# Kernel tuning notes

Measured on AMD Instinct MI355X. Metric: run time of the kernel, lower is better.

Reference implementation:

```python
import math
import jax, jax.numpy as jnp
import numpy as np

N_HEADS = 16

def setup_inputs() -> dict:
    key = jax.random.key(0)
    k1, k2, k3 = jax.random.split(key, 3)
    B, T, C = 2, 2048, 1024
    x = jax.random.normal(k1, (B, T, C), dtype=jnp.float32)
    # Linear weights stored as [in, out] so y = x @ W + b (same math as torch Linear)
    w_qkv = jax.random.normal(k2, (C, 3 * C), dtype=jnp.float32) * (1.0 / math.sqrt(C))
    b_qkv = jnp.zeros((3 * C,), dtype=jnp.float32)
    w_out = jax.random.normal(k3, (C, C), dtype=jnp.float32) * (1.0 / math.sqrt(C))
    b_out = jnp.zeros((C,), dtype=jnp.float32)
    return {"x": x, "w_qkv": w_qkv, "b_qkv": b_qkv, "w_out": w_out, "b_out": b_out}

def reference(x, w_qkv, b_qkv, w_out, b_out):
    B, T, C = x.shape
    H = N_HEADS
    hd = C // H
    qkv = (x @ w_qkv + b_qkv).reshape(B, T, 3, H, hd)
    q, k, v = qkv[:, :, 0], qkv[:, :, 1], qkv[:, :, 2]  # [B,T,H,hd]
    scale = 1.0 / math.sqrt(hd)
    att = jnp.einsum('bqhd,bkhd->bhqk', q, k) * scale  # [B,H,T,T]
    causal = jnp.tril(jnp.ones((T, T), dtype=bool))
    att = jnp.where(causal[None, None], att, jnp.float32(-jnp.inf))
    att = jax.nn.softmax(att, axis=-1)
    # dropout p=0.0 -> identity (eval mode)
    y = jnp.einsum('bhqk,bkhd->bqhd', att, v).reshape(B, T, C)
    return y @ w_out + b_out
```

## Files before the change

kernel.cpp:

```cpp
#include <hip/hip_runtime.h>
#include <hip/hip_bf16.h>
#include <stdint.h>


typedef __bf16 bf16_t;
typedef __attribute__((ext_vector_type(8))) __bf16 bf16x8;
typedef __attribute__((ext_vector_type(4))) __bf16 bf16x4;
typedef __attribute__((ext_vector_type(4))) short short4v;
typedef __attribute__((ext_vector_type(4))) float f32x4;

static_assert(sizeof(bf16x8) == 16, "bf16x8 must be 16B");

#if defined(__has_builtin)
#if __has_builtin(__builtin_amdgcn_mfma_f32_16x16x16bf16_1k)
#define HAVE_MFMA16 1
#endif
#if __has_builtin(__builtin_amdgcn_exp2f)
#define EXP2F(x) __builtin_amdgcn_exp2f(x)
#endif
#endif
#ifndef HAVE_MFMA16
#define HAVE_MFMA16 0
#endif
#ifndef EXP2F
#define EXP2F(x) exp2f(x)
#endif

__device__ inline void async_copy16(const bf16_t* gsrc, bf16_t* lds_dst) {
  __builtin_amdgcn_global_load_lds(
      (const __attribute__((address_space(1))) uint32_t*)(const void*)gsrc,
      (__attribute__((address_space(3))) uint32_t*)(void*)lds_dst,
      16, 0, 0);
}

__global__ __launch_bounds__(256) void prep_kernel(
    const float* __restrict__ x, const float* __restrict__ wq,
    const float* __restrict__ wo, bf16_t* __restrict__ xb,
    bf16_t* __restrict__ wqkvT, bf16_t* __restrict__ woutT) {
  __shared__ bf16_t tile[32][33];
  const int bid = blockIdx.x;
  if (bid < 2048) {
    const int i = bid * 256 + threadIdx.x;
    const float4* s = (const float4*)x;
    float4 a = s[i * 2], b = s[i * 2 + 1];
    bf16x8 o;
    o[0] = (bf16_t)a.x; o[1] = (bf16_t)a.y; o[2] = (bf16_t)a.z; o[3] = (bf16_t)a.w;
    o[4] = (bf16_t)b.x; o[5] = (bf16_t)b.y; o[6] = (bf16_t)b.z; o[7] = (bf16_t)b.w;
    ((bf16x8*)xb)[i] = o;
    return;
  }
  const bool isq = bid < 5120;
  const int id = isq ? bid - 2048 : bid - 5120;
  const int C = isq ? 3072 : 1024;
  const int R = 1024;
  const int nbx = isq ? 96 : 32;
  const float* in = isq ? wq : wo;
  bf16_t* out = isq ? wqkvT : woutT;
  const int c0 = (id % nbx) * 32, r0 = (id / nbx) * 32;
  const int tx4 = threadIdx.x & 7;
  const int ty = threadIdx.x >> 3;
  {
    const float4 ld =
        *(const float4*)&in[(size_t)(r0 + ty) * C + c0 + tx4 * 4];
    tile[ty][tx4 * 4 + 0] = (bf16_t)ld.x;
    tile[ty][tx4 * 4 + 1] = (bf16_t)ld.y;
    tile[ty][tx4 * 4 + 2] = (bf16_t)ld.z;
    tile[ty][tx4 * 4 + 3] = (bf16_t)ld.w;
  }
  __syncthreads();
  {
    bf16x4 w;
    w[0] = tile[tx4 * 4 + 0][ty];
    w[1] = tile[tx4 * 4 + 1][ty];
    w[2] = tile[tx4 * 4 + 2][ty];
    w[3] = tile[tx4 * 4 + 3][ty];
    *(bf16x4*)&out[(size_t)(c0 + ty) * R + r0 + tx4 * 4] = w;
  }
}

template <bool OUT_F32>
__global__ __launch_bounds__(256, 3) void gemm_bt_kernel(
    const bf16_t* __restrict__ A, const bf16_t* __restrict__ Bt,
    const float* __restrict__ bias, void* __restrict__ Cv, int M, int N,
    int K) {
  __shared__ __align__(16) bf16_t sA[128 * 64];
  __shared__ __align__(16) bf16_t sB[128 * 64];
  const int tid = threadIdx.x;
  const int wave = tid >> 6, lane = tid & 63;
  const int quad = lane >> 4, l16 = lane & 15;
  const int wm = (wave >> 1) * 64, wn = (wave & 1) * 64;
  const int bm = blockIdx.y * 128, bn = blockIdx.x * 128;

  const int rl = lane >> 3, cl = lane & 7;
  const int srow = wave * 32;
  const bf16_t* gA =
      A + (size_t)(bm + srow + rl) * K + (size_t)((cl ^ rl) << 3);
  const bf16_t* gB =
      Bt + (size_t)(bn + srow + rl) * K + (size_t)((cl ^ rl) << 3);
  bf16_t* lA = sA + srow * 64;
  bf16_t* lB = sB + srow * 64;

  f32x4 acc[4][4] = {};

  for (int k0 = 0; k0 < K; k0 += 64) {
    __syncthreads();
#pragma unroll
    for (int c = 0; c < 4; c++) {
      async_copy16(gA + (size_t)(c * 8) * K + k0, lA + c * 512);
      async_copy16(gB + (size_t)(c * 8) * K + k0, lB + c * 512);
    }
    __syncthreads();

#pragma unroll
    for (int h = 0; h < 2; h++) {
      bf16x8 af[4], bfr[4];
#pragma unroll
      for (int i = 0; i < 4; i++) {
        const int row = wm + i * 16 + l16;
        af[i] = *(const bf16x8*)&sA[row * 64 +
                                    (((h * 4 + quad) ^ (row & 7)) << 3)];
      }
#pragma unroll
      for (int j = 0; j < 4; j++) {
        const int row = wn + j * 16 + l16;
        bfr[j] = *(const bf16x8*)&sB[row * 64 +
                                     (((h * 4 + quad) ^ (row & 7)) << 3)];
      }
#pragma unroll
      for (int i = 0; i < 4; i++)
#pragma unroll
        for (int j = 0; j < 4; j++)
          acc[i][j] = __builtin_amdgcn_mfma_f32_16x16x32_bf16(
              af[i], bfr[j], acc[i][j], 0, 0, 0);
    }
  }

#pragma unroll
  for (int j = 0; j < 4; j++) {
    const int col = bn + wn + j * 16 + l16;
    const float bv = bias[col];
#pragma unroll
    for (int i = 0; i < 4; i++) {
#pragma unroll
      for (int r = 0; r < 4; r++) {
        const int row = bm + wm + i * 16 + quad * 4 + r;
        const float v = acc[i][j][r] + bv;
        if (OUT_F32)
          ((float*)Cv)[(size_t)row * N + col] = v;
        else
          ((bf16_t*)Cv)[(size_t)row * N + col] = (bf16_t)v;
      }
    }
  }
}

__global__ __launch_bounds__(256) void gemm_bt64_kernel(
    const bf16_t* __restrict__ A, const bf16_t* __restrict__ Bt,
    const float* __restrict__ bias, float* __restrict__ C, int M, int N,
    int K) {
  __shared__ __align__(16) bf16_t sA[64 * 64];
  __shared__ __align__(16) bf16_t sB[128 * 64];
  const int tid = threadIdx.x;
  const int wave = tid >> 6, lane = tid & 63;
  const int quad = lane >> 4, l16 = lane & 15;
  const int wm = (wave >> 1) * 32, wn = (wave & 1) * 64;
  const int bm = blockIdx.y * 64, bn = blockIdx.x * 128;

  const int rl = lane >> 3, cl = lane & 7;
  const bf16_t* gA =
      A + (size_t)(bm + wave * 16 + rl) * K + (size_t)((cl ^ rl) << 3);
  bf16_t* lA = sA + (wave * 16) * 64;
  const bf16_t* gB =
      Bt + (size_t)(bn + wave * 32 + rl) * K + (size_t)((cl ^ rl) << 3);
  bf16_t* lB = sB + (wave * 32) * 64;

  f32x4 acc[2][4] = {};

  for (int k0 = 0; k0 < K; k0 += 64) {
    __syncthreads();
#pragma unroll
    for (int c = 0; c < 2; c++)
      async_copy16(gA + (size_t)(c * 8) * K + k0, lA + c * 512);
#pragma unroll
    for (int c = 0; c < 4; c++)
      async_copy16(gB + (size_t)(c * 8) * K + k0, lB + c * 512);
    __syncthreads();

#pragma unroll
    for (int h = 0; h < 2; h++) {
      bf16x8 af[2], bfr[4];
#pragma unroll
      for (int i = 0; i < 2; i++) {
        const int row = wm + i * 16 + l16;
        af[i] = *(const bf16x8*)&sA[row * 64 +
                                    (((h * 4 + quad) ^ (row & 7)) << 3)];
      }
#pragma unroll
      for (int j = 0; j < 4; j++) {
        const int row = wn + j * 16 + l16;
        bfr[j] = *(const bf16x8*)&sB[row * 64 +
                                     (((h * 4 + quad) ^ (row & 7)) << 3)];
      }
#pragma unroll
      for (int i = 0; i < 2; i++)
#pragma unroll
        for (int j = 0; j < 4; j++)
          acc[i][j] = __builtin_amdgcn_mfma_f32_16x16x32_bf16(
              af[i], bfr[j], acc[i][j], 0, 0, 0);
    }
  }

#pragma unroll
  for (int j = 0; j < 4; j++) {
    const int col = bn + wn + j * 16 + l16;
    const float bv = bias[col];
#pragma unroll
    for (int i = 0; i < 2; i++) {
#pragma unroll
      for (int r = 0; r < 4; r++) {
        const int row = bm + wm + i * 16 + quad * 4 + r;
        C[(size_t)row * N + col] = acc[i][j][r] + bv;
      }
    }
  }
}

#if HAVE_MFMA16
__global__ __launch_bounds__(256, 4) void attn_kernel(
    const bf16_t* __restrict__ qkv, bf16_t* __restrict__ Y) {
  constexpr int T = 2048, C3 = 3072;
  constexpr float CSC = 0.18033688f;
  constexpr float MB = 20.0f;
  __shared__ __align__(16) bf16_t sK[2][64 * 64];
  __shared__ __align__(16) bf16_t sVt[2][64 * 64];

  const int tid = threadIdx.x;
  const int wave = tid >> 6, lane = tid & 63;
  const int quad = lane >> 4, l16 = lane & 15;
  const int bh = blockIdx.y;
  const int flip = (bh >> 3) & 1;
  const int vv = ((int)blockIdx.x + ((bh >> 4) & 1) * 8) & 31;
  const int X = flip ? (31 - vv) : vv;
  const int q0 = X * 64;
  const int b = bh >> 4, h = bh & 15;
  const size_t base = (size_t)b * T * C3 + (size_t)h * 64;

  const int qrow = q0 + wave * 16 + l16;
  const bf16x8 qf0 = *(const bf16x8*)&qkv[base + (size_t)qrow * C3 + quad * 8];
  const bf16x8 qf1 =
      *(const bf16x8*)&qkv[base + (size_t)qrow * C3 + 32 + quad * 8];

  f32x4 o[4] = {};
  f32x4 l4 = {0.f, 0.f, 0.f, 0.f};

  const int t = tid >> 2, seg = tid & 3;
  const bf16_t* gK = &qkv[base + (size_t)t * C3 + 1024 + seg * 16];
  const int kq = tid >> 4, dq = tid & 15;
  const bf16_t* gV = &qkv[base + (size_t)(4 * kq) * C3 + 2048 + dq * 4];

  bf16x8 kr0 = *(const bf16x8*)gK;
  bf16x8 kr1 = *(const bf16x8*)(gK + 8);
  bf16x4 vA0 = *(const bf16x4*)gV;
  bf16x4 vA1 = *(const bf16x4*)(gV + C3);
  bf16x4 vA2 = *(const bf16x4*)(gV + 2 * C3);
  bf16x4 vA3 = *(const bf16x4*)(gV + 3 * C3);

  for (int kt = 0; kt < X; kt++) {
    const int p = kt & 1;
    *(bf16x8*)&sK[p][t * 64 + (((2 * seg + 0) ^ (t & 7)) << 3)] = kr0;
    *(bf16x8*)&sK[p][t * 64 + (((2 * seg + 1) ^ (t & 7)) << 3)] = kr1;
#pragma unroll
    for (int i = 0; i < 4; i++) {
      const int d = dq * 4 + i;
      bf16x4 w;
      w[0] = vA0[i]; w[1] = vA1[i]; w[2] = vA2[i]; w[3] = vA3[i];
      *(bf16x4*)&sVt[p][d * 64 + ((kq ^ (d & 15)) << 2)] = w;
    }
    {
      const size_t off = (size_t)(kt + 1) * 64 * C3;
      kr0 = *(const bf16x8*)(gK + off);
      kr1 = *(const bf16x8*)(gK + off + 8);
      vA0 = *(const bf16x4*)(gV + off);
      vA1 = *(const bf16x4*)(gV + off + C3);
      vA2 = *(const bf16x4*)(gV + off + 2 * C3);
      vA3 = *(const bf16x4*)(gV + off + 3 * C3);
    }
    __syncthreads();

#pragma unroll
    for (int j = 0; j < 4; j++) {
      const int trow = j * 16 + l16;
      bf16x8 kf0 =
          *(const bf16x8*)&sK[p][trow * 64 + ((quad ^ (trow & 7)) << 3)];
      bf16x8 kf1 =
          *(const bf16x8*)&sK[p][trow * 64 + (((4 + quad) ^ (trow & 7)) << 3)];
      f32x4 s2 = {};
      __builtin_amdgcn_s_setprio(1);
      s2 = __builtin_amdgcn_mfma_f32_16x16x32_bf16(kf0, qf0, s2, 0, 0, 0);
      s2 = __builtin_amdgcn_mfma_f32_16x16x32_bf16(kf1, qf1, s2, 0, 0, 0);
      __builtin_amdgcn_s_setprio(0);
#pragma unroll
      for (int r = 0; r < 4; r++) s2[r] = EXP2F(fmaf(s2[r], CSC, -MB));
      l4 += s2;
      bf16x4 pb;
      pb[0] = (bf16_t)s2[0]; pb[1] = (bf16_t)s2[1];
      pb[2] = (bf16_t)s2[2]; pb[3] = (bf16_t)s2[3];
      union { bf16x4 bv; short4v sv; } u;
      u.bv = pb;
      const short4v pa = u.sv;
      __builtin_amdgcn_s_setprio(1);
#pragma unroll
      for (int n16 = 0; n16 < 4; n16++) {
        const int d = n16 * 16 + l16;
        const short4v vf = *(const short4v*)&sVt[p][d * 64 +
                                                    (((j * 4 + quad) ^ (d & 15))
                                                     << 2)];
        o[n16] =
            __builtin_amdgcn_mfma_f32_16x16x16bf16_1k(pa, vf, o[n16], 0, 0, 0);
      }
      __builtin_amdgcn_s_setprio(0);
    }
  }

  {
    const int p = X & 1;
    *(bf16x8*)&sK[p][t * 64 + (((2 * seg + 0) ^ (t & 7)) << 3)] = kr0;
    *(bf16x8*)&sK[p][t * 64 + (((2 * seg + 1) ^ (t & 7)) << 3)] = kr1;
#pragma unroll
    for (int i = 0; i < 4; i++) {
      const int d = dq * 4 + i;
      bf16x4 w;
      w[0] = vA0[i]; w[1] = vA1[i]; w[2] = vA2[i]; w[3] = vA3[i];
      *(bf16x4*)&sVt[p][d * 64 + ((kq ^ (d & 15)) << 2)] = w;
    }
    __syncthreads();

#pragma unroll
    for (int j = 0; j < 4; j++) {
      if (j > wave) continue;
      const int trow = j * 16 + l16;
      bf16x8 kf0 =
          *(const bf16x8*)&sK[p][trow * 64 + ((quad ^ (trow & 7)) << 3)];
      bf16x8 kf1 =
          *(const bf16x8*)&sK[p][trow * 64 + (((4 + quad) ^ (trow & 7)) << 3)];
      f32x4 s2 = {};
      __builtin_amdgcn_s_setprio(1);
      s2 = __builtin_amdgcn_mfma_f32_16x16x32_bf16(kf0, qf0, s2, 0, 0, 0);
      s2 = __builtin_amdgcn_mfma_f32_16x16x32_bf16(kf1, qf1, s2, 0, 0, 0);
      __builtin_amdgcn_s_setprio(0);
      const bool diag = (j == wave);
#pragma unroll
      for (int r = 0; r < 4; r++) {
        float pv = EXP2F(fmaf(s2[r], CSC, -MB));
        if (diag && (quad * 4 + r > l16)) pv = 0.f;
        s2[r] = pv;
      }
      l4 += s2;
      bf16x4 pb;
      pb[0] = (bf16_t)s2[0]; pb[1] = (bf16_t)s2[1];
      pb[2] = (bf16_t)s2[2]; pb[3] = (bf16_t)s2[3];
      union { bf16x4 bv; short4v sv; } u;
      u.bv = pb;
      const short4v pa = u.sv;
      __builtin_amdgcn_s_setprio(1);
#pragma unroll
      for (int n16 = 0; n16 < 4; n16++) {
        const int d = n16 * 16 + l16;
        const short4v vf = *(const short4v*)&sVt[p][d * 64 +
                                                    (((j * 4 + quad) ^ (d & 15))
                                                     << 2)];
        o[n16] =
            __builtin_amdgcn_mfma_f32_16x16x16bf16_1k(pa, vf, o[n16], 0, 0, 0);
      }
      __builtin_amdgcn_s_setprio(0);
    }
  }

  float l_acc = (l4[0] + l4[1]) + (l4[2] + l4[3]);
  l_acc += __shfl_xor(l_acc, 16);
  l_acc += __shfl_xor(l_acc, 32);
#pragma unroll
  for (int r = 0; r < 4; r++) {
    const float lr = __shfl(l_acc, quad * 4 + r);
    const float inv = 1.0f / lr;
    const int row = q0 + wave * 16 + quad * 4 + r;
#pragma unroll
    for (int n16 = 0; n16 < 4; n16++)
      Y[((size_t)b * T + row) * 1024 + h * 64 + n16 * 16 + l16] =
          (bf16_t)(o[n16][r] * inv);
  }
}
#else
__global__ __launch_bounds__(256, 4) void attn_kernel(
    const bf16_t* __restrict__ qkv, bf16_t* __restrict__ Y) {
  constexpr int T = 2048, C3 = 3072;
  constexpr float CSC = 0.18033688f;
  constexpr float MB = 20.0f;
  __shared__ __align__(16) bf16_t sK[64 * 64];
  __shared__ __align__(16) bf16_t sVt[64 * 64];
  __shared__ __align__(16) bf16_t sP[4][16 * 64];

  const int tid = threadIdx.x;
  const int wave = tid >> 6, lane = tid & 63;
  const int quad = lane >> 4, l16 = lane & 15;
  const int bh = blockIdx.y;
  const int flip = (bh >> 3) & 1;
  const int vv = ((int)blockIdx.x + ((bh >> 4) & 1) * 8) & 31;
  const int X = flip ? (31 - vv) : vv;
  const int q0 = X * 64;
  const int b = bh >> 4, h = bh & 15;
  const size_t base = (size_t)b * T * C3 + (size_t)h * 64;

  const int qrow = q0 + wave * 16 + l16;
  const bf16x8 qf0 = *(const bf16x8*)&qkv[base + (size_t)qrow * C3 + quad * 8];
  const bf16x8 qf1 =
      *(const bf16x8*)&qkv[base + (size_t)qrow * C3 + 32 + quad * 8];

  f32x4 o[4] = {};
  float l_i[4] = {0.f, 0.f, 0.f, 0.f};

  const int t = tid >> 2, seg = tid & 3;
  const int tk = t & 7, tg3 = t >> 3;
  const bf16_t* gK = &qkv[base + (size_t)t * C3 + 1024 + seg * 16];
  const bf16_t* gV = &qkv[base + (size_t)t * C3 + 2048 + seg * 16];

  const int ktiles = X + 1;

  bf16x8 kr0 = *(const bf16x8*)gK;
  bf16x8 kr1 = *(const bf16x8*)(gK + 8);
  bf16x8 vr0 = *(const bf16x8*)gV;
  bf16x8 vr1 = *(const bf16x8*)(gV + 8);

  for (int kt = 0; kt < ktiles; kt++) {
    __syncthreads();
    *(bf16x8*)&sK[t * 64 + (((2 * seg + 0) ^ tk) << 3)] = kr0;
    *(bf16x8*)&sK[t * 64 + (((2 * seg + 1) ^ tk) << 3)] = kr1;
#pragma unroll
    for (int i = 0; i < 8; i++) {
      const int d = seg * 16 + i;
      sVt[d * 64 + ((tg3 ^ (d >> 3)) << 3) + (t & 7)] = vr0[i];
    }
#pragma unroll
    for (int i = 0; i < 8; i++) {
      const int d = seg * 16 + 8 + i;
      sVt[d * 64 + ((tg3 ^ (d >> 3)) << 3) + (t & 7)] = vr1[i];
    }
    __syncthreads();

    if (kt + 1 < ktiles) {
      const size_t off = (size_t)(kt + 1) * 64 * C3;
      kr0 = *(const bf16x8*)(gK + off);
      kr1 = *(const bf16x8*)(gK + off + 8);
      vr0 = *(const bf16x8*)(gV + off);
      vr1 = *(const bf16x8*)(gV + off + 8);
    }

    f32x4 s[4] = {};
#pragma unroll
    for (int j = 0; j < 4; j++) {
      const int kkey = l16 & 7;
      bf16x8 kf0 =
          *(const bf16x8*)&sK[(j * 16 + l16) * 64 + ((quad ^ kkey) << 3)];
      bf16x8 kf1 =
          *(const bf16x8*)&sK[(j * 16 + l16) * 64 + (((4 + quad) ^ kkey) << 3)];
      s[j] = __builtin_amdgcn_mfma_f32_16x16x32_bf16(qf0, kf0, s[j], 0, 0, 0);
      s[j] = __builtin_amdgcn_mfma_f32_16x16x32_bf16(qf1, kf1, s[j], 0, 0, 0);
    }

#pragma unroll
    for (int j = 0; j < 4; j++)
#pragma unroll
      for (int r = 0; r < 4; r++) s[j][r] = EXP2F(fmaf(s[j][r], CSC, -MB));
    if (kt == ktiles - 1) {
      const int k0 = kt * 64;
#pragma unroll
      for (int j = 0; j < 4; j++) {
        const int kcol = k0 + j * 16 + l16;
#pragma unroll
        for (int r = 0; r < 4; r++)
          if (kcol > q0 + wave * 16 + quad * 4 + r) s[j][r] = 0.f;
      }
    }
#pragma unroll
    for (int j = 0; j < 4; j++)
#pragma unroll
      for (int r = 0; r < 4; r++) l_i[r] += s[j][r];

    bf16_t* sp = &sP[wave][0];
#pragma unroll
    for (int j = 0; j < 4; j++)
#pragma unroll
      for (int r = 0; r < 4; r++) {
        const int m = quad * 4 + r;
        const int kw = (m + (m >> 3)) & 7;
        sp[m * 64 + ((((2 * j + (l16 >> 3)) ^ kw)) << 3) + (l16 & 7)] =
            (bf16_t)s[j][r];
      }

    const int kap = (l16 + (l16 >> 3)) & 7;
#pragma unroll
    for (int s2 = 0; s2 < 2; s2++) {
      bf16x8 pf =
          *(const bf16x8*)&sp[l16 * 64 + (((4 * s2 + quad) ^ kap) << 3)];
#pragma unroll
      for (int j = 0; j < 4; j++) {
        const int d = j * 16 + l16;
        bf16x8 vf =
            *(const bf16x8*)&sVt[d * 64 + (((4 * s2 + quad) ^ (d >> 3)) << 3)];
        o[j] = __builtin_amdgcn_mfma_f32_16x16x32_bf16(pf, vf, o[j], 0, 0, 0);
      }
    }
  }

#pragma unroll
  for (int r = 0; r < 4; r++) {
    float l = l_i[r];
#pragma unroll
    for (int off = 1; off < 16; off <<= 1) l += __shfl_xor(l, off);
    const float inv = 1.0f / l;
    const int row = q0 + wave * 16 + quad * 4 + r;
#pragma unroll
    for (int j = 0; j < 4; j++)
      Y[((size_t)b * T + row) * 1024 + h * 64 + j * 16 + l16] =
          (bf16_t)(o[j][r] * inv);
  }
}
#endif

extern "C" void kernel_launch(void* const* d_in, const int* in_sizes, int n_in,
                              void* d_out, int out_size, void* d_ws,
                              size_t ws_size, hipStream_t stream) {
  const float* x = nullptr;
  const float* w_qkv = nullptr;
  const float* b_qkv = nullptr;
  const float* w_out = nullptr;
  const float* b_out = nullptr;
  for (int i = 0; i < n_in; i++) {
    switch (in_sizes[i]) {
      case 4194304: x = (const float*)d_in[i]; break;
      case 3145728: w_qkv = (const float*)d_in[i]; break;
      case 3072:    b_qkv = (const float*)d_in[i]; break;
      case 1048576: w_out = (const float*)d_in[i]; break;
      case 1024:    b_out = (const float*)d_in[i]; break;
      default: break;
    }
  }
  float* out = (float*)d_out;

  bf16_t* xb = (bf16_t*)d_ws;
  bf16_t* wqkvT = xb + (size_t)4194304;
  bf16_t* woutT = wqkvT + (size_t)3145728;
  bf16_t* qkv = woutT + (size_t)1048576;
  bf16_t* Y = qkv + (size_t)12582912;

  prep_kernel<<<6144, 256, 0, stream>>>(x, w_qkv, w_out, xb, wqkvT, woutT);
  gemm_bt_kernel<false><<<dim3(24, 32), 256, 0, stream>>>(
      xb, wqkvT, b_qkv, (void*)qkv, 4096, 3072, 1024);
  attn_kernel<<<dim3(32, 32), 256, 0, stream>>>(qkv, Y);
  gemm_bt64_kernel<<<dim3(8, 64), 256, 0, stream>>>(
      Y, woutT, b_out, out, 4096, 1024, 1024);
}
```

Measured before the change: 171.9 us.

## Split attention key tiles across wave pairs with 512-thread blocks

The attention kernel now runs 8 waves per block, two per 16-row query slice, and each wave of a pair handles half of the 64 key columns in every tile. Partial outputs and row sums from the second wave are merged through LDS before normalization. K and V staging is split by role, with half the threads loading K and the other half loading V. The aim is to shorten each wave's serial dependence chain and raise occupancy. The cost is an extra LDS reduction, more barriers per block, and half as many MFMAs per wave to hide latency. The non-MFMA fallback kernel is removed.

```diff
diff --git a/kernel.cpp b/kernel.cpp
--- a/kernel.cpp
+++ b/kernel.cpp
@@ -12,15 +12,9 @@
 static_assert(sizeof(bf16x8) == 16, "bf16x8 must be 16B");
 
 #if defined(__has_builtin)
-#if __has_builtin(__builtin_amdgcn_mfma_f32_16x16x16bf16_1k)
-#define HAVE_MFMA16 1
-#endif
 #if __has_builtin(__builtin_amdgcn_exp2f)
 #define EXP2F(x) __builtin_amdgcn_exp2f(x)
 #endif
-#endif
-#ifndef HAVE_MFMA16
-#define HAVE_MFMA16 0
 #endif
 #ifndef EXP2F
 #define EXP2F(x) exp2f(x)
@@ -225,8 +219,7 @@
   }
 }
 
-#if HAVE_MFMA16
-__global__ __launch_bounds__(256, 4) void attn_kernel(
+__global__ __launch_bounds__(512, 8) void attn_kernel(
     const bf16_t* __restrict__ qkv, bf16_t* __restrict__ Y) {
   constexpr int T = 2048, C3 = 3072;
   constexpr float CSC = 0.18033688f;
@@ -237,6 +230,8 @@
   const int tid = threadIdx.x;
   const int wave = tid >> 6, lane = tid & 63;
   const int quad = lane >> 4, l16 = lane & 15;
+  const int wq = wave >> 1;
+  const int jh = wave & 1;
   const int bh = blockIdx.y;
   const int flip = (bh >> 3) & 1;
   const int vv = ((int)blockIdx.x + ((bh >> 4) & 1) * 8) & 31;
@@ -245,7 +240,7 @@
   const int b = bh >> 4, h = bh & 15;
   const size_t base = (size_t)b * T * C3 + (size_t)h * 64;
 
-  const int qrow = q0 + wave * 16 + l16;
+  const int qrow = q0 + wq * 16 + l16;
   const bf16x8 qf0 = *(const bf16x8*)&qkv[base + (size_t)qrow * C3 + quad * 8];
   const bf16x8 qf1 =
       *(const bf16x8*)&qkv[base + (size_t)qrow * C3 + 32 + quad * 8];
@@ -253,42 +248,55 @@
   f32x4 o[4] = {};
   f32x4 l4 = {0.f, 0.f, 0.f, 0.f};
 
-  const int t = tid >> 2, seg = tid & 3;
-  const bf16_t* gK = &qkv[base + (size_t)t * C3 + 1024 + seg * 16];
-  const int kq = tid >> 4, dq = tid & 15;
+  const bool krole = tid < 256;
+  const int st = (tid & 255) >> 2, sseg = tid & 3;
+  const bf16_t* gK = &qkv[base + (size_t)st * C3 + 1024 + sseg * 16];
+  const int kq = (tid & 255) >> 4, dq = tid & 15;
   const bf16_t* gV = &qkv[base + (size_t)(4 * kq) * C3 + 2048 + dq * 4];
 
-  bf16x8 kr0 = *(const bf16x8*)gK;
-  bf16x8 kr1 = *(const bf16x8*)(gK + 8);
-  bf16x4 vA0 = *(const bf16x4*)gV;
-  bf16x4 vA1 = *(const bf16x4*)(gV + C3);
-  bf16x4 vA2 = *(const bf16x4*)(gV + 2 * C3);
-  bf16x4 vA3 = *(const bf16x4*)(gV + 3 * C3);
+  bf16x8 kr0 = {}, kr1 = {};
+  bf16x4 vA0 = {}, vA1 = {}, vA2 = {}, vA3 = {};
+  if (krole) {
+    kr0 = *(const bf16x8*)gK;
+    kr1 = *(const bf16x8*)(gK + 8);
+  } else {
+    vA0 = *(const bf16x4*)gV;
+    vA1 = *(const bf16x4*)(gV + C3);
+    vA2 = *(const bf16x4*)(gV + 2 * C3);
+    vA3 = *(const bf16x4*)(gV + 3 * C3);
+  }
 
   for (int kt = 0; kt < X; kt++) {
     const int p = kt & 1;
-    *(bf16x8*)&sK[p][t * 64 + (((2 * seg + 0) ^ (t & 7)) << 3)] = kr0;
-    *(bf16x8*)&sK[p][t * 64 + (((2 * seg + 1) ^ (t & 7)) << 3)] = kr1;
-#pragma unroll
-    for (int i = 0; i < 4; i++) {
-      const int d = dq * 4 + i;
-      bf16x4 w;
-      w[0] = vA0[i]; w[1] = vA1[i]; w[2] = vA2[i]; w[3] = vA3[i];
-      *(bf16x4*)&sVt[p][d * 64 + ((kq ^ (d & 15)) << 2)] = w;
+    if (krole) {
+      *(bf16x8*)&sK[p][st * 64 + (((2 * sseg + 0) ^ (st & 7)) << 3)] = kr0;
+      *(bf16x8*)&sK[p][st * 64 + (((2 * sseg + 1) ^ (st & 7)) << 3)] = kr1;
+    } else {
+#pragma unroll
+      for (int i = 0; i < 4; i++) {
+        const int d = dq * 4 + i;
+        bf16x4 w;
+        w[0] = vA0[i]; w[1] = vA1[i]; w[2] = vA2[i]; w[3] = vA3[i];
+        *(bf16x4*)&sVt[p][d * 64 + ((kq ^ (d & 15)) << 2)] = w;
+      }
     }
     {
       const size_t off = (size_t)(kt + 1) * 64 * C3;
-      kr0 = *(const bf16x8*)(gK + off);
-      kr1 = *(const bf16x8*)(gK + off + 8);
-      vA0 = *(const bf16x4*)(gV + off);
-      vA1 = *(const bf16x4*)(gV + off + C3);
-      vA2 = *(const bf16x4*)(gV + off + 2 * C3);
-      vA3 = *(const bf16x4*)(gV + off + 3 * C3);
-    }
-    __syncthreads();
-
-#pragma unroll
-    for (int j = 0; j < 4; j++) {
+      if (krole) {
+        kr0 = *(const bf16x8*)(gK + off);
+        kr1 = *(const bf16x8*)(gK + off + 8);
+      } else {
+        vA0 = *(const bf16x4*)(gV + off);
+        vA1 = *(const bf16x4*)(gV + off + C3);
+        vA2 = *(const bf16x4*)(gV + off + 2 * C3);
+        vA3 = *(const bf16x4*)(gV + off + 3 * C3);
+      }
+    }
+    __syncthreads();
+
+#pragma unroll
+    for (int jj = 0; jj < 2; jj++) {
+      const int j = jh * 2 + jj;
       const int trow = j * 16 + l16;
       bf16x8 kf0 =
           *(const bf16x8*)&sK[p][trow * 64 + ((quad ^ (trow & 7)) << 3)];
@@ -324,20 +332,24 @@
 
   {
     const int p = X & 1;
-    *(bf16x8*)&sK[p][t * 64 + (((2 * seg + 0) ^ (t & 7)) << 3)] = kr0;
-    *(bf16x8*)&sK[p][t * 64 + (((2 * seg + 1) ^ (t & 7)) << 3)] = kr1;
-#pragma unroll
-    for (int i = 0; i < 4; i++) {
-      const int d = dq * 4 + i;
-      bf16x4 w;
-      w[0] = vA0[i]; w[1] = vA1[i]; w[2] = vA2[i]; w[3] = vA3[i];
-      *(bf16x4*)&sVt[p][d * 64 + ((kq ^ (d & 15)) << 2)] = w;
-    }
-    __syncthreads();
-
-#pragma unroll
-    for (int j = 0; j < 4; j++) {
-      if (j > wave) continue;
+    if (krole) {
+      *(bf16x8*)&sK[p][st * 64 + (((2 * sseg + 0) ^ (st & 7)) << 3)] = kr0;
+      *(bf16x8*)&sK[p][st * 64 + (((2 * sseg + 1) ^ (st & 7)) << 3)] = kr1;
+    } else {
+#pragma unroll
+      for (int i = 0; i < 4; i++) {
+        const int d = dq * 4 + i;
+        bf16x4 w;
+        w[0] = vA0[i]; w[1] = vA1[i]; w[2] = vA2[i]; w[3] = vA3[i];
+        *(bf16x4*)&sVt[p][d * 64 + ((kq ^ (d & 15)) << 2)] = w;
+      }
+    }
+    __syncthreads();
+
+#pragma unroll
+    for (int jj = 0; jj < 2; jj++) {
+      const int j = jh * 2 + jj;
+      if (j > wq) continue;
       const int trow = j * 16 + l16;
       bf16x8 kf0 =
           *(const bf16x8*)&sK[p][trow * 64 + ((quad ^ (trow & 7)) << 3)];
@@ -348,7 +360,7 @@
       s2 = __builtin_amdgcn_mfma_f32_16x16x32_bf16(kf0, qf0, s2, 0, 0, 0);
       s2 = __builtin_amdgcn_mfma_f32_16x16x32_bf16(kf1, qf1, s2, 0, 0, 0);
       __builtin_amdgcn_s_setprio(0);
-      const bool diag = (j == wave);
+      const bool diag = (j == wq);
 #pragma unroll
       for (int r = 0; r < 4; r++) {
         float pv = EXP2F(fmaf(s2[r], CSC, -MB));
@@ -379,153 +391,34 @@
   float l_acc = (l4[0] + l4[1]) + (l4[2] + l4[3]);
   l_acc += __shfl_xor(l_acc, 16);
   l_acc += __shfl_xor(l_acc, 32);
-#pragma unroll
-  for (int r = 0; r < 4; r++) {
-    const float lr = __shfl(l_acc, quad * 4 + r);
-    const float inv = 1.0f / lr;
-    const int row = q0 + wave * 16 + quad * 4 + r;
-#pragma unroll
-    for (int n16 = 0; n16 < 4; n16++)
-      Y[((size_t)b * T + row) * 1024 + h * 64 + n16 * 16 + l16] =
-          (bf16_t)(o[n16][r] * inv);
-  }
-}
-#else
-__global__ __launch_bounds__(256, 4) void attn_kernel(
-    const bf16_t* __restrict__ qkv, bf16_t* __restrict__ Y) {
-  constexpr int T = 2048, C3 = 3072;
-  constexpr float CSC = 0.18033688f;
-  constexpr float MB = 20.0f;
-  __shared__ __align__(16) bf16_t sK[64 * 64];
-  __shared__ __align__(16) bf16_t sVt[64 * 64];
-  __shared__ __align__(16) bf16_t sP[4][16 * 64];
-
-  const int tid = threadIdx.x;
-  const int wave = tid >> 6, lane = tid & 63;
-  const int quad = lane >> 4, l16 = lane & 15;
-  const int bh = blockIdx.y;
-  const int flip = (bh >> 3) & 1;
-  const int vv = ((int)blockIdx.x + ((bh >> 4) & 1) * 8) & 31;
-  const int X = flip ? (31 - vv) : vv;
-  const int q0 = X * 64;
-  const int b = bh >> 4, h = bh & 15;
-  const size_t base = (size_t)b * T * C3 + (size_t)h * 64;
-
-  const int qrow = q0 + wave * 16 + l16;
-  const bf16x8 qf0 = *(const bf16x8*)&qkv[base + (size_t)qrow * C3 + quad * 8];
-  const bf16x8 qf1 =
-      *(const bf16x8*)&qkv[base + (size_t)qrow * C3 + 32 + quad * 8];
-
-  f32x4 o[4] = {};
-  float l_i[4] = {0.f, 0.f, 0.f, 0.f};
-
-  const int t = tid >> 2, seg = tid & 3;
-  const int tk = t & 7, tg3 = t >> 3;
-  const bf16_t* gK = &qkv[base + (size_t)t * C3 + 1024 + seg * 16];
-  const bf16_t* gV = &qkv[base + (size_t)t * C3 + 2048 + seg * 16];
-
-  const int ktiles = X + 1;
-
-  bf16x8 kr0 = *(const bf16x8*)gK;
-  bf16x8 kr1 = *(const bf16x8*)(gK + 8);
-  bf16x8 vr0 = *(const bf16x8*)gV;
-  bf16x8 vr1 = *(const bf16x8*)(gV + 8);
-
-  for (int kt = 0; kt < ktiles; kt++) {
-    __syncthreads();
-    *(bf16x8*)&sK[t * 64 + (((2 * seg + 0) ^ tk) << 3)] = kr0;
-    *(bf16x8*)&sK[t * 64 + (((2 * seg + 1) ^ tk) << 3)] = kr1;
-#pragma unroll
-    for (int i = 0; i < 8; i++) {
-      const int d = seg * 16 + i;
-      sVt[d * 64 + ((tg3 ^ (d >> 3)) << 3) + (t & 7)] = vr0[i];
-    }
-#pragma unroll
-    for (int i = 0; i < 8; i++) {
-      const int d = seg * 16 + 8 + i;
-      sVt[d * 64 + ((tg3 ^ (d >> 3)) << 3) + (t & 7)] = vr1[i];
-    }
-    __syncthreads();
-
-    if (kt + 1 < ktiles) {
-      const size_t off = (size_t)(kt + 1) * 64 * C3;
-      kr0 = *(const bf16x8*)(gK + off);
-      kr1 = *(const bf16x8*)(gK + off + 8);
-      vr0 = *(const bf16x8*)(gV + off);
-      vr1 = *(const bf16x8*)(gV + off + 8);
-    }
-
-    f32x4 s[4] = {};
-#pragma unroll
-    for (int j = 0; j < 4; j++) {
-      const int kkey = l16 & 7;
-      bf16x8 kf0 =
-          *(const bf16x8*)&sK[(j * 16 + l16) * 64 + ((quad ^ kkey) << 3)];
-      bf16x8 kf1 =
-          *(const bf16x8*)&sK[(j * 16 + l16) * 64 + (((4 + quad) ^ kkey) << 3)];
-      s[j] = __builtin_amdgcn_mfma_f32_16x16x32_bf16(qf0, kf0, s[j], 0, 0, 0);
-      s[j] = __builtin_amdgcn_mfma_f32_16x16x32_bf16(qf1, kf1, s[j], 0, 0, 0);
-    }
-
-#pragma unroll
-    for (int j = 0; j < 4; j++)
-#pragma unroll
-      for (int r = 0; r < 4; r++) s[j][r] = EXP2F(fmaf(s[j][r], CSC, -MB));
-    if (kt == ktiles - 1) {
-      const int k0 = kt * 64;
-#pragma unroll
-      for (int j = 0; j < 4; j++) {
-        const int kcol = k0 + j * 16 + l16;
-#pragma unroll
-        for (int r = 0; r < 4; r++)
-          if (kcol > q0 + wave * 16 + quad * 4 + r) s[j][r] = 0.f;
-      }
-    }
-#pragma unroll
-    for (int j = 0; j < 4; j++)
-#pragma unroll
-      for (int r = 0; r < 4; r++) l_i[r] += s[j][r];
-
-    bf16_t* sp = &sP[wave][0];
-#pragma unroll
-    for (int j = 0; j < 4; j++)
-#pragma unroll
-      for (int r = 0; r < 4; r++) {
-        const int m = quad * 4 + r;
-        const int kw = (m + (m >> 3)) & 7;
-        sp[m * 64 + ((((2 * j + (l16 >> 3)) ^ kw)) << 3) + (l16 & 7)] =
-            (bf16_t)s[j][r];
-      }
-
-    const int kap = (l16 + (l16 >> 3)) & 7;
-#pragma unroll
-    for (int s2 = 0; s2 < 2; s2++) {
-      bf16x8 pf =
-          *(const bf16x8*)&sp[l16 * 64 + (((4 * s2 + quad) ^ kap) << 3)];
-#pragma unroll
-      for (int j = 0; j < 4; j++) {
-        const int d = j * 16 + l16;
-        bf16x8 vf =
-            *(const bf16x8*)&sVt[d * 64 + (((4 * s2 + quad) ^ (d >> 3)) << 3)];
-        o[j] = __builtin_amdgcn_mfma_f32_16x16x32_bf16(pf, vf, o[j], 0, 0, 0);
-      }
-    }
-  }
-
-#pragma unroll
-  for (int r = 0; r < 4; r++) {
-    float l = l_i[r];
-#pragma unroll
-    for (int off = 1; off < 16; off <<= 1) l += __shfl_xor(l, off);
-    const float inv = 1.0f / l;
-    const int row = q0 + wave * 16 + quad * 4 + r;
-#pragma unroll
-    for (int j = 0; j < 4; j++)
-      Y[((size_t)b * T + row) * 1024 + h * 64 + j * 16 + l16] =
-          (bf16_t)(o[j][r] * inv);
-  }
-}
-#endif
+
+  __syncthreads();
+  float* mo = (float*)&sK[0][0];
+  float* ml = (float*)&sVt[0][0];
+  if (jh == 1) {
+    float* dst = mo + ((size_t)(wq * 64 + lane)) * 16;
+#pragma unroll
+    for (int n16 = 0; n16 < 4; n16++) *(f32x4*)(dst + n16 * 4) = o[n16];
+    if (quad == 0) ml[wq * 16 + l16] = l_acc;
+  }
+  __syncthreads();
+  if (jh == 0) {
+    const float* src = mo + ((size_t)(wq * 64 + lane)) * 16;
+#pragma unroll
+    for (int n16 = 0; n16 < 4; n16++) o[n16] += *(const f32x4*)(src + n16 * 4);
+    const float lsum = l_acc + ml[wq * 16 + l16];
+#pragma unroll
+    for (int r = 0; r < 4; r++) {
+      const float lr = __shfl(lsum, quad * 4 + r);
+      const float inv = 1.0f / lr;
+      const int row = q0 + wq * 16 + quad * 4 + r;
+#pragma unroll
+      for (int n16 = 0; n16 < 4; n16++)
+        Y[((size_t)b * T + row) * 1024 + h * 64 + n16 * 16 + l16] =
+            (bf16_t)(o[n16][r] * inv);
+    }
+  }
+}
 
 extern "C" void kernel_launch(void* const* d_in, const int* in_sizes, int n_in,
                               void* d_out, int out_size, void* d_ws,
@@ -556,7 +449,7 @@
   prep_kernel<<<6144, 256, 0, stream>>>(x, w_qkv, w_out, xb, wqkvT, woutT);
   gemm_bt_kernel<false><<<dim3(24, 32), 256, 0, stream>>>(
       xb, wqkvT, b_qkv, (void*)qkv, 4096, 3072, 1024);
-  attn_kernel<<<dim3(32, 32), 256, 0, stream>>>(qkv, Y);
+  attn_kernel<<<dim3(32, 32), 512, 0, stream>>>(qkv, Y);
   gemm_bt64_kernel<<<dim3(8, 64), 256, 0, stream>>>(
       Y, woutT, b_out, out, 4096, 1024, 1024);
 }
```

New measurement: 222.5 us. 29.5% more time.
